# Optimization experiments

Measured on AMD Instinct MI355X. Metric: run time of the kernel, lower is better.

Reference implementation:

```python
import jax, jax.numpy as jnp
import numpy as np

KERNEL_SIZE = 3   # init kwarg kernel_size
BATCHSIZE = 4     # init kwarg batchsize (true output batch; bs = num * BATCHSIZE)


def setup_inputs() -> dict:
    key = jax.random.key(0)
    k1, k2, k3 = jax.random.split(key, 3)
    num = 4                      # candidate flows per image
    bs = num * BATCHSIZE         # 16
    ds, hs, ws = 256, 64, 64
    hf, wf = 64, 64
    source = jax.random.normal(k1, (bs, ds, hs, ws), dtype=jnp.float32)
    # flows with realistic magnitude (a few pixels of displacement)
    flow_field = jax.random.normal(k2, (bs, 2, hf, wf), dtype=jnp.float32) * 8.0
    masks = jax.random.uniform(k3, (bs, 1, hf, wf), dtype=jnp.float32)
    return {"source": source, "flow_field": flow_field, "masks": masks}


def _bilinear_sample_zero(img, y, x):
    """img: (C,H,W); y,x: (Ho,Wo) continuous coords. Zero outside bounds."""
    C, H, W = img.shape
    y0 = jnp.floor(y).astype(jnp.int32)
    x0 = jnp.floor(x).astype(jnp.int32)
    out = jnp.zeros((C,) + y.shape, img.dtype)
    for dy in (0, 1):
        for dx in (0, 1):
            yi = y0 + dy
            xi = x0 + dx
            w = (1.0 - jnp.abs(y - yi)) * (1.0 - jnp.abs(x - xi))
            valid = (yi >= 0) & (yi < H) & (xi >= 0) & (xi < W)
            v = img[:, jnp.clip(yi, 0, H - 1), jnp.clip(xi, 0, W - 1)]  # (C,Ho,Wo)
            out = out + jnp.where(valid, w, 0.0)[None] * v
    return out


def reference(source, flow_field, masks):
    k, B = KERNEL_SIZE, BATCHSIZE
    bs, ds, hs, ws = source.shape
    hf, wf = flow_field.shape[2], flow_field.shape[3]
    num = bs // B
    Ho, Wo = k * hf, k * wf

    ys = jnp.arange(Ho)
    xs = jnp.arange(Wo)
    ysrc = ys // k              # which flow cell each output row belongs to
    xsrc = xs // k
    yoff = (ys % k) - (k // 2)  # centered in-block offset
    xoff = (xs % k) - (k // 2)

    # expand per-cell flow to per-output-pixel: (bs, Ho, Wo)
    fy = flow_field[:, 0][:, ysrc][:, :, xsrc]
    fx = flow_field[:, 1][:, ysrc][:, :, xsrc]
    py = ysrc.astype(fy.dtype)[:, None] + yoff.astype(fy.dtype)[:, None] + fy
    px = xsrc.astype(fx.dtype)[None, :] + xoff.astype(fx.dtype)[None, :] + fx

    sampled = jax.vmap(_bilinear_sample_zero)(source, py, px)  # (bs, ds, Ho, Wo)

    # per-cell mask broadcast over the kxk block and channels
    m = masks[:, :, ysrc][:, :, :, xsrc]  # (bs, 1, Ho, Wo)
    weighted = sampled * m

    # accumulate the num candidate flows into the true batch
    out = weighted.reshape(num, B, ds, Ho, Wo).sum(axis=0)
    return out
```

## Files before the change

kernel.cpp:

```cpp
#include <hip/hip_runtime.h>

#define DS 256
#define HS 64
#define WS 64
#define BOUT 4
#define NUM 4
#define HO 192
#define WO 192
#define NT 512
#define ROWDW 36
#define IMGDW (HS * ROWDW)

__device__ __forceinline__ unsigned int f2bf(float f) {
    unsigned int u = __float_as_uint(f);
    return (u + 0x7fffu + ((u >> 16) & 1u)) >> 16;
}

__global__ __launch_bounds__(NT, 4)
void mbe_kernel(const float* __restrict__ src,
                const float* __restrict__ flow,
                const float* __restrict__ masks,
                float* __restrict__ out)
{
    __shared__ unsigned int img[NUM * IMGDW];

    const int d  = blockIdx.x;
    const int bo = blockIdx.y;
    const int tid = threadIdx.x;

    if (tid < NUM * HS) {
        const int n = tid >> 6, row = tid & 63;
        unsigned int* rb = img + n * IMGDW + row * ROWDW;
        *(uint2*)rb        = make_uint2(0u, 0u);
        *(uint2*)(rb + 34) = make_uint2(0u, 0u);
    }

    #pragma unroll
    for (int l = 0; l < 4; ++l) {
        const int s = l * NT + tid;
        const int n = s >> 9, row = (s >> 3) & 63, seg = s & 7;
        const float* g = src + (((size_t)((n * BOUT + bo) * DS + d)) << 12) + (row << 6) + (seg << 3);
        const float4 a = *(const float4*)g;
        const float4 b = *(const float4*)(g + 4);
        const unsigned int p0 = f2bf(a.x) | (f2bf(a.y) << 16);
        const unsigned int p1 = f2bf(a.z) | (f2bf(a.w) << 16);
        const unsigned int p2 = f2bf(b.x) | (f2bf(b.y) << 16);
        const unsigned int p3 = f2bf(b.z) | (f2bf(b.w) << 16);
        unsigned int* dst = img + n * IMGDW + row * ROWDW + 2 + (seg << 2);
        *(uint2*)dst       = make_uint2(p0, p1);
        *(uint2*)(dst + 2) = make_uint2(p2, p3);
    }
    __syncthreads();

    const size_t obase = ((size_t)bo * DS + d) * (size_t)(HO * WO);

    #pragma unroll 1
    for (int it = 0; it < 8; ++it) {
        const int g  = it * NT + tid;
        const int ys = g >> 6;
        const int xs = g & 63;

        float fy[NUM], fx[NUM], mm[NUM];
        #pragma unroll
        for (int n = 0; n < NUM; ++n) {
            const int b = n * BOUT + bo;
            fy[n] = flow[((size_t)(b * 2 + 0) << 12) + g];
            fx[n] = flow[((size_t)(b * 2 + 1) << 12) + g];
            mm[n] = masks[((size_t)b << 12) + g];
        }

        float acc[3][3];
        #pragma unroll
        for (int j = 0; j < 3; ++j)
            #pragma unroll
            for (int i = 0; i < 3; ++i)
                acc[j][i] = 0.0f;

        #pragma unroll
        for (int n = 0; n < NUM; ++n) {
            const float gy = (float)ys + fy[n];
            const float gx = (float)xs + fx[n];
            const float fiy = floorf(gy);
            const float fix = floorf(gx);
            const int iy = (int)fiy;
            const int ix = (int)fix;
            const float ty = gy - fiy;
            const float tx = gx - fix;

            const int xb = ix - 1;
            int c0 = xb & ~3;
            c0 = min(max(c0, -4), 60);
            const int r = xb - c0;
            const bool rhi = (r >= 2);
            const unsigned int sh = (unsigned int)((r & 1) << 4);

            const float omtx = 1.0f - tx;
            const float A0 = ((unsigned)xb       < (unsigned)WS) ? omtx : 0.0f;
            const float A1 = ((unsigned)(xb + 1) < (unsigned)WS) ? omtx : 0.0f;
            const float A2 = ((unsigned)(xb + 2) < (unsigned)WS) ? omtx : 0.0f;
            const float B0 = ((unsigned)(xb + 1) < (unsigned)WS) ? tx : 0.0f;
            const float B1 = ((unsigned)(xb + 2) < (unsigned)WS) ? tx : 0.0f;
            const float B2 = ((unsigned)(xb + 3) < (unsigned)WS) ? tx : 0.0f;

            const float wy1 = mm[n] * ty;
            const float wy0 = mm[n] - wy1;
            float WA[3], WB[3];
            #pragma unroll
            for (int j = 0; j < 3; ++j) {
                WA[j] = ((unsigned)(iy - 1 + j) < (unsigned)HS) ? wy0 : 0.0f;
                WB[j] = ((unsigned)(iy + j)     < (unsigned)HS) ? wy1 : 0.0f;
            }

            const unsigned int* imgn = img + n * IMGDW;
            const int cdw = (c0 >> 1) + 2;

            #pragma unroll
            for (int rr = 0; rr < 4; ++rr) {
                const int yy = iy - 1 + rr;
                const int yyc = min(max(yy, 0), HS - 1);
                const unsigned int* p = imgn + yyc * ROWDW + cdw;
                const uint2 u01 = *(const uint2*)p;
                const uint2 u23 = *(const uint2*)(p + 2);
                const unsigned int X = rhi ? u01.y : u01.x;
                const unsigned int Y = rhi ? u23.x : u01.y;
                const unsigned int Z = rhi ? u23.y : u23.x;
                const unsigned int A = __builtin_amdgcn_alignbit(Y, X, sh);
                const unsigned int B = __builtin_amdgcn_alignbit(Z, Y, sh);
                const float v0 = __uint_as_float(A << 16);
                const float v1 = __uint_as_float(A & 0xffff0000u);
                const float v2 = __uint_as_float(B << 16);
                const float v3 = __uint_as_float(B & 0xffff0000u);
                const float h0 = v0 * A0 + v1 * B0;
                const float h1 = v1 * A1 + v2 * B1;
                const float h2 = v2 * A2 + v3 * B2;
                if (rr <= 2) {
                    acc[rr][0] += WA[rr] * h0;
                    acc[rr][1] += WA[rr] * h1;
                    acc[rr][2] += WA[rr] * h2;
                }
                if (rr >= 1) {
                    acc[rr - 1][0] += WB[rr - 1] * h0;
                    acc[rr - 1][1] += WB[rr - 1] * h1;
                    acc[rr - 1][2] += WB[rr - 1] * h2;
                }
            }
        }

        #pragma unroll
        for (int j = 0; j < 3; ++j) {
            const int yo = 3 * ys + j;
            #pragma unroll
            for (int i = 0; i < 3; ++i) {
                const int xo = 3 * xs + i;
                out[obase + (size_t)yo * WO + xo] = acc[j][i];
            }
        }
    }
}

extern "C" void kernel_launch(void* const* d_in, const int* in_sizes, int n_in,
                              void* d_out, int out_size, void* d_ws, size_t ws_size,
                              hipStream_t stream) {
    const float* src   = (const float*)d_in[0];
    const float* flow  = (const float*)d_in[1];
    const float* masks = (const float*)d_in[2];
    float* out = (float*)d_out;

    dim3 grid(DS, BOUT);
    mbe_kernel<<<grid, NT, 0, stream>>>(src, flow, masks, out);
}
```

Baseline: 235.7 us.

## Use odd-stride padded LDS rows with clamped x and implicit zero borders

Changes the shared-memory row stride to an odd 37 dwords and widens the zero padding to 2 dwords left and 3 right. Clamping x with fmed3 lets out-of-range horizontal taps read zeros from the padding instead of computing per-tap validity weights. Horizontal interpolation becomes a single lerp, and the image is read with three scalar dword loads instead of two 64-bit loads plus selects. The odd stride is meant to reduce LDS bank conflicts, at the cost of splitting vector LDS writes into scalar ones and a slower division-based zero-fill loop.

```diff
diff --git a/kernel.cpp b/kernel.cpp
--- a/kernel.cpp
+++ b/kernel.cpp
@@ -8,7 +8,7 @@
 #define HO 192
 #define WO 192
 #define NT 512
-#define ROWDW 36
+#define ROWDW 37
 #define IMGDW (HS * ROWDW)
 
 __device__ __forceinline__ unsigned int f2bf(float f) {
@@ -28,11 +28,13 @@
     const int bo = blockIdx.y;
     const int tid = threadIdx.x;
 
-    if (tid < NUM * HS) {
-        const int n = tid >> 6, row = tid & 63;
-        unsigned int* rb = img + n * IMGDW + row * ROWDW;
-        *(uint2*)rb        = make_uint2(0u, 0u);
-        *(uint2*)(rb + 34) = make_uint2(0u, 0u);
+    for (int idx = tid; idx < NUM * HS * 5; idx += NT) {
+        const int n   = idx / (HS * 5);
+        const int r   = idx - n * (HS * 5);
+        const int row = r / 5;
+        const int c5  = r - row * 5;
+        const int dw  = (c5 < 2) ? c5 : (c5 + 32);
+        img[n * IMGDW + row * ROWDW + dw] = 0u;
     }
 
     #pragma unroll
@@ -47,8 +49,7 @@
         const unsigned int p2 = f2bf(b.x) | (f2bf(b.y) << 16);
         const unsigned int p3 = f2bf(b.z) | (f2bf(b.w) << 16);
         unsigned int* dst = img + n * IMGDW + row * ROWDW + 2 + (seg << 2);
-        *(uint2*)dst       = make_uint2(p0, p1);
-        *(uint2*)(dst + 2) = make_uint2(p2, p3);
+        dst[0] = p0; dst[1] = p1; dst[2] = p2; dst[3] = p3;
     }
     __syncthreads();
 
@@ -79,28 +80,18 @@
         #pragma unroll
         for (int n = 0; n < NUM; ++n) {
             const float gy = (float)ys + fy[n];
-            const float gx = (float)xs + fx[n];
+            const float gxc = __builtin_amdgcn_fmed3f((float)xs + fx[n], -3.0f, 66.0f);
+
+            const float fix = floorf(gxc);
+            const int   ix  = (int)fix;
+            const float tx  = gxc - fix;
+            const int   xb  = ix - 1;
+            const unsigned int sh = (unsigned int)((xb & 1) << 4);
+            const int   cdw = (xb >> 1) + 2;
+
             const float fiy = floorf(gy);
-            const float fix = floorf(gx);
-            const int iy = (int)fiy;
-            const int ix = (int)fix;
-            const float ty = gy - fiy;
-            const float tx = gx - fix;
-
-            const int xb = ix - 1;
-            int c0 = xb & ~3;
-            c0 = min(max(c0, -4), 60);
-            const int r = xb - c0;
-            const bool rhi = (r >= 2);
-            const unsigned int sh = (unsigned int)((r & 1) << 4);
-
-            const float omtx = 1.0f - tx;
-            const float A0 = ((unsigned)xb       < (unsigned)WS) ? omtx : 0.0f;
-            const float A1 = ((unsigned)(xb + 1) < (unsigned)WS) ? omtx : 0.0f;
-            const float A2 = ((unsigned)(xb + 2) < (unsigned)WS) ? omtx : 0.0f;
-            const float B0 = ((unsigned)(xb + 1) < (unsigned)WS) ? tx : 0.0f;
-            const float B1 = ((unsigned)(xb + 2) < (unsigned)WS) ? tx : 0.0f;
-            const float B2 = ((unsigned)(xb + 3) < (unsigned)WS) ? tx : 0.0f;
+            const int   iy  = (int)fiy;
+            const float ty  = gy - fiy;
 
             const float wy1 = mm[n] * ty;
             const float wy0 = mm[n] - wy1;
@@ -112,27 +103,24 @@
             }
 
             const unsigned int* imgn = img + n * IMGDW;
-            const int cdw = (c0 >> 1) + 2;
 
             #pragma unroll
             for (int rr = 0; rr < 4; ++rr) {
-                const int yy = iy - 1 + rr;
+                const int yy  = iy - 1 + rr;
                 const int yyc = min(max(yy, 0), HS - 1);
                 const unsigned int* p = imgn + yyc * ROWDW + cdw;
-                const uint2 u01 = *(const uint2*)p;
-                const uint2 u23 = *(const uint2*)(p + 2);
-                const unsigned int X = rhi ? u01.y : u01.x;
-                const unsigned int Y = rhi ? u23.x : u01.y;
-                const unsigned int Z = rhi ? u23.y : u23.x;
+                const unsigned int X = p[0];
+                const unsigned int Y = p[1];
+                const unsigned int Z = p[2];
                 const unsigned int A = __builtin_amdgcn_alignbit(Y, X, sh);
                 const unsigned int B = __builtin_amdgcn_alignbit(Z, Y, sh);
                 const float v0 = __uint_as_float(A << 16);
                 const float v1 = __uint_as_float(A & 0xffff0000u);
                 const float v2 = __uint_as_float(B << 16);
                 const float v3 = __uint_as_float(B & 0xffff0000u);
-                const float h0 = v0 * A0 + v1 * B0;
-                const float h1 = v1 * A1 + v2 * B1;
-                const float h2 = v2 * A2 + v3 * B2;
+                const float h0 = v0 + tx * (v1 - v0);
+                const float h1 = v1 + tx * (v2 - v1);
+                const float h2 = v2 + tx * (v3 - v2);
                 if (rr <= 2) {
                     acc[rr][0] += WA[rr] * h0;
                     acc[rr][1] += WA[rr] * h1;
```

New measurement: 233.0 us. About the same (-1.1%).
